# Performance work log

Hardware: AMD Instinct MI355X
Metric: run time of the kernel (lower is better)

The kernel has to match this reference:

```python
import jax, jax.numpy as jnp
import numpy as np

B, T, HID = 2, 1024, 1024
H, DK, DV = 16, 64, 64
K = 4            # short conv kernel size
CG = 15          # CG iterations (max_cg_step_training)
EPS = 1e-5       # norm_eps


def setup_inputs() -> dict:
    key = jax.random.key(0)
    ks = jax.random.split(key, 12)
    s = 1.0 / np.sqrt(HID)
    nrm = lambda k, sh, sc: (jax.random.normal(k, sh, jnp.float32) * sc)
    hidden_states = nrm(ks[0], (B, T, HID), 1.0)
    Wq = nrm(ks[1], (HID, HID), s)
    Wk = nrm(ks[2], (HID, HID), s)
    Wv = nrm(ks[3], (HID, HID), s)
    Wa = nrm(ks[4], (HID, H), s)
    Wb = nrm(ks[5], (HID, H), s)
    bb = jnp.zeros((H,), jnp.float32)
    A_log = jnp.log(jax.random.uniform(ks[6], (H,), jnp.float32, 1e-3, 16.0))
    dt = jnp.exp(jax.random.uniform(ks[7], (H,), jnp.float32) * (np.log(0.1) - np.log(0.001)) + np.log(0.001))
    dt = jnp.clip(dt, 1e-4)
    dt_bias = dt + jnp.log(-jnp.expm1(-dt))
    lam_init = float(np.log(np.exp(1.0 - 0.25) - 1.0))
    lambda_params = jnp.full((HID,), lam_init, jnp.float32)
    Wconv_q = nrm(ks[8], (HID, K), 0.3)
    Wconv_k = nrm(ks[9], (HID, K), 0.3)
    norm_w = jnp.ones((DV,), jnp.float32)
    Wo = nrm(ks[10], (HID, HID), s)
    return dict(hidden_states=hidden_states, Wq=Wq, Wk=Wk, Wv=Wv, Wa=Wa, Wb=Wb, bb=bb,
                A_log=A_log, dt_bias=dt_bias, lambda_params=lambda_params,
                Wconv_q=Wconv_q, Wconv_k=Wconv_k, norm_w=norm_w, Wo=Wo)


def _short_conv(x, w):
    # causal depthwise conv1d + silu. x: [b,t,c], w: [c,K]
    t = x.shape[1]
    xp = jnp.pad(x, ((0, 0), (K - 1, 0), (0, 0)))
    y = sum(xp[:, i:i + t, :] * w[:, i] for i in range(K))
    return jax.nn.silu(y)


def _l2norm(x):
    return x * jax.lax.rsqrt(jnp.sum(x * x, -1, keepdims=True) + 1e-6)


def _forward(hidden_states, Wq, Wk, Wv, Wa, Wb, bb, A_log, dt_bias, lambda_params, Wconv_q, Wconv_k, norm_w, Wo):
    b, t, _ = hidden_states.shape
    q = _short_conv(hidden_states @ Wq, Wconv_q)
    k = _short_conv(hidden_states @ Wk, Wconv_k)
    v = hidden_states @ Wv
    q = _l2norm(q.reshape(b, t, H, DK))
    k = _l2norm(k.reshape(b, t, H, DK))
    v = v.reshape(b, t, H, DV)
    beta = jax.nn.sigmoid(hidden_states @ Wb + bb)                         # [b,t,h]
    g = -jnp.exp(A_log) * jax.nn.softplus(hidden_states @ Wa + dt_bias)    # [b,t,h]
    lamb = jax.nn.softplus(lambda_params).reshape(H, DK) + 0.25            # [h,dk]

    def cg_solve(Hkk, rhs):
        # solve (Hkk + diag(lamb)) x = rhs, fixed-iteration CG, batched over [b,h]
        mv = lambda p: jnp.einsum('bhij,bhj->bhi', Hkk, p) + lamb * p
        x = jnp.zeros_like(rhs)
        r = rhs
        p = r
        rs = jnp.sum(r * r, -1, keepdims=True)
        for _ in range(CG):
            Ap = mv(p)
            alpha = rs / (jnp.sum(p * Ap, -1, keepdims=True) + 1e-12)
            x = x + alpha * p
            r = r - alpha * Ap
            rs_new = jnp.sum(r * r, -1, keepdims=True)
            p = r + (rs_new / (rs + 1e-12)) * p
            rs = rs_new
        return x

    def step(carry, inp):
        Hkk, Hkv = carry
        qt, kt, vt, gt, bt = inp
        decay = jnp.exp(gt)[..., None, None]
        w = bt[..., None, None]
        Hkk = decay * Hkk + w * (kt[..., :, None] * kt[..., None, :])
        Hkv = decay * Hkv + w * (kt[..., :, None] * vt[..., None, :])
        x = cg_solve(Hkk, qt)
        o = jnp.einsum('bhi,bhij->bhj', x, Hkv)
        return (Hkk, Hkv), o

    qT = q.transpose(1, 0, 2, 3)
    kT = k.transpose(1, 0, 2, 3)
    vT = v.transpose(1, 0, 2, 3)
    gT = g.transpose(1, 0, 2)
    bT = beta.transpose(1, 0, 2)
    Hkk0 = jnp.zeros((b, H, DK, DK), hidden_states.dtype)
    Hkv0 = jnp.zeros((b, H, DK, DV), hidden_states.dtype)
    _, oT = jax.lax.scan(jax.checkpoint(step), (Hkk0, Hkv0), (qT, kT, vT, gT, bT))
    o = oT.transpose(1, 0, 2, 3)                                           # [b,t,h,dv]
    o = o * jax.lax.rsqrt(jnp.mean(o * o, -1, keepdims=True) + EPS) * norm_w
    return o.reshape(b, t, H * DV) @ Wo


def reference(hidden_states, Wq, Wk, Wv, Wa, Wb, bb, A_log, dt_bias, lambda_params, Wconv_q, Wconv_k, norm_w, Wo):
    return _forward(hidden_states, Wq, Wk, Wv, Wa, Wb, bb, A_log, dt_bias, lambda_params, Wconv_q, Wconv_k, norm_w, Wo)
```

## Files before the change

kernel.cpp:

```cpp
#include <hip/hip_runtime.h>
#include <hip/hip_bf16.h>
#include <stdint.h>

#define T_LEN 1024
#define HIDN  1024
#define NH    16
#define DKV   64
#define KCONV 4
#define CG_IT 15
#define CC    32
#define NC    (T_LEN / CC)
#define PAD   68

typedef __attribute__((ext_vector_type(8))) short          bf16x8;
typedef __attribute__((ext_vector_type(8))) unsigned short u16x8;
typedef __attribute__((ext_vector_type(4))) unsigned short u16x4;
typedef __attribute__((ext_vector_type(4))) float          f32x4;

__device__ __forceinline__ float softplusf(float x) {
    return x > 20.f ? x : log1pf(expf(x));
}
__device__ __forceinline__ unsigned short f2bf(float x) {
    __hip_bfloat16 b = __float2bfloat16(x);
    return *reinterpret_cast<unsigned short*>(&b);
}
__device__ __forceinline__ bf16x8 pack8(float4 a, float4 b) {
    union { bf16x8 v; unsigned short u[8]; } r;
    r.u[0] = f2bf(a.x); r.u[1] = f2bf(a.y); r.u[2] = f2bf(a.z); r.u[3] = f2bf(a.w);
    r.u[4] = f2bf(b.x); r.u[5] = f2bf(b.y); r.u[6] = f2bf(b.z); r.u[7] = f2bf(b.w);
    return r.v;
}

__global__ __launch_bounds__(256) void cast_bf16(const float* __restrict__ src,
                                                 unsigned short* __restrict__ dst,
                                                 int n4)
{
    int i = blockIdx.x * 256 + threadIdx.x;
    if (i >= n4) return;
    float4 v = *reinterpret_cast<const float4*>(src + (size_t)i * 4);
    u16x4 o;
    o.x = f2bf(v.x); o.y = f2bf(v.y); o.z = f2bf(v.z); o.w = f2bf(v.w);
    *reinterpret_cast<u16x4*>(dst + (size_t)i * 4) = o;
}

__global__ __launch_bounds__(256) void transpose_cast(const float* __restrict__ W,
                                                      unsigned short* __restrict__ WT,
                                                      int K, int N)
{
    __shared__ unsigned short sT[64][68];
    int n0 = blockIdx.x * 64, k0 = blockIdx.y * 64;
    int tid = threadIdx.x;
    int rr = tid >> 4, cc4 = (tid & 15) * 4;
#pragma unroll
    for (int p = 0; p < 4; p++) {
        int r = p * 16 + rr;
        float4 v = *reinterpret_cast<const float4*>(&W[(size_t)(k0 + r) * N + n0 + cc4]);
        sT[cc4 + 0][r] = f2bf(v.x);
        sT[cc4 + 1][r] = f2bf(v.y);
        sT[cc4 + 2][r] = f2bf(v.z);
        sT[cc4 + 3][r] = f2bf(v.w);
    }
    __syncthreads();
#pragma unroll
    for (int p = 0; p < 4; p++) {
        int r = p * 16 + rr;
        u16x4 v = *reinterpret_cast<const u16x4*>(&sT[r][cc4]);
        *reinterpret_cast<u16x4*>(&WT[(size_t)(n0 + r) * K + k0 + cc4]) = v;
    }
}

__global__ __launch_bounds__(256) void gemm_bf16(const unsigned short* __restrict__ A,
                                                 const unsigned short* __restrict__ Bt,
                                                 float* __restrict__ C,
                                                 int M, int N, int K)
{
    __shared__ unsigned short sA[64][40];
    __shared__ unsigned short sB[64][40];
    const int tid = threadIdx.x;
    const int bm = blockIdx.y * 64, bn = blockIdx.x * 64;
    const int w = tid >> 6, lane = tid & 63;
    const int l16 = lane & 15, quad = lane >> 4;
    const int lrow = tid >> 2, lk = (tid & 3) * 8;

    f32x4 acc[4];
#pragma unroll
    for (int f = 0; f < 4; f++) acc[f] = (f32x4){0.f, 0.f, 0.f, 0.f};

    const size_t arow = (size_t)(bm + lrow) * K;
    const size_t brow = (size_t)(bn + lrow) * K;

    for (int k0 = 0; k0 < K; k0 += 32) {
        u16x8 av = *reinterpret_cast<const u16x8*>(A + arow + k0 + lk);
        u16x8 bv = *reinterpret_cast<const u16x8*>(Bt + brow + k0 + lk);
        *reinterpret_cast<u16x8*>(&sA[lrow][lk]) = av;
        *reinterpret_cast<u16x8*>(&sB[lrow][lk]) = bv;
        __syncthreads();

        bf16x8 aF = *reinterpret_cast<const bf16x8*>(&sA[w * 16 + l16][quad * 8]);
#pragma unroll
        for (int f = 0; f < 4; f++) {
            bf16x8 bF = *reinterpret_cast<const bf16x8*>(&sB[f * 16 + l16][quad * 8]);
            acc[f] = __builtin_amdgcn_mfma_f32_16x16x32_bf16(aF, bF, acc[f], 0, 0, 0);
        }
        __syncthreads();
    }

#pragma unroll
    for (int f = 0; f < 4; f++) {
#pragma unroll
        for (int i = 0; i < 4; i++) {
            int m = bm + w * 16 + quad * 4 + i;
            C[(size_t)m * N + bn + f * 16 + l16] = acc[f][i];
        }
    }
}

__global__ __launch_bounds__(256) void gemm_qkv(const unsigned short* __restrict__ A,
                                                const unsigned short* __restrict__ Bt,
                                                float* __restrict__ C)
{
    const int K = 1024;
    __shared__ unsigned short sA[64][40];
    __shared__ unsigned short sB[64][40];
    const int tid = threadIdx.x;
    const int bm = blockIdx.y * 64, bn = blockIdx.x * 64;
    const int mat = bn >> 10, n0 = bn & 1023;
    const int w = tid >> 6, lane = tid & 63;
    const int l16 = lane & 15, quad = lane >> 4;
    const int lrow = tid >> 2, lk = (tid & 3) * 8;

    f32x4 acc[4];
#pragma unroll
    for (int f = 0; f < 4; f++) acc[f] = (f32x4){0.f, 0.f, 0.f, 0.f};

    const size_t arow = (size_t)(bm + lrow) * K;
    const size_t brow = (size_t)(bn + lrow) * K;

    for (int k0 = 0; k0 < K; k0 += 32) {
        u16x8 av = *reinterpret_cast<const u16x8*>(A + arow + k0 + lk);
        u16x8 bv = *reinterpret_cast<const u16x8*>(Bt + brow + k0 + lk);
        *reinterpret_cast<u16x8*>(&sA[lrow][lk]) = av;
        *reinterpret_cast<u16x8*>(&sB[lrow][lk]) = bv;
        __syncthreads();

        bf16x8 aF = *reinterpret_cast<const bf16x8*>(&sA[w * 16 + l16][quad * 8]);
#pragma unroll
        for (int f = 0; f < 4; f++) {
            bf16x8 bF = *reinterpret_cast<const bf16x8*>(&sB[f * 16 + l16][quad * 8]);
            acc[f] = __builtin_amdgcn_mfma_f32_16x16x32_bf16(aF, bF, acc[f], 0, 0, 0);
        }
        __syncthreads();
    }

    float* Cb = C + (size_t)mat * (2048u * 1024u);
#pragma unroll
    for (int f = 0; f < 4; f++) {
#pragma unroll
        for (int i = 0; i < 4; i++) {
            int m = bm + w * 16 + quad * 4 + i;
            Cb[(size_t)m * 1024 + n0 + f * 16 + l16] = acc[f][i];
        }
    }
}

__global__ __launch_bounds__(256) void proj_gb(const float* __restrict__ hidden,
                                               const float* __restrict__ Wa,
                                               const float* __restrict__ Wb,
                                               const float* __restrict__ bb,
                                               const float* __restrict__ A_log,
                                               const float* __restrict__ dt_bias,
                                               float* __restrict__ g_out,
                                               float* __restrict__ beta_out)
{
    int idx = blockIdx.x * 256 + threadIdx.x;
    int row = idx >> 4, h = idx & 15;
    const float* hr = hidden + (size_t)row * HIDN;
    float da = 0.f, db = 0.f;
    for (int i = 0; i < HIDN; i++) {
        float x = hr[i];
        da += x * Wa[i * NH + h];
        db += x * Wb[i * NH + h];
    }
    float sp = softplusf(da + dt_bias[h]);
    g_out[idx]    = -expf(A_log[h]) * sp;
    beta_out[idx] = 1.f / (1.f + expf(-(db + bb[h])));
}

__global__ __launch_bounds__(1024) void cumsum_g(const float* __restrict__ g_in,
                                                 const float* __restrict__ beta_in,
                                                 float* __restrict__ G_out,
                                                 float* __restrict__ betaT)
{
    __shared__ float s[1024];
    int bh = blockIdx.x;
    int b = bh >> 4, h = bh & 15;
    int t = threadIdx.x;
    size_t src = ((size_t)(b * T_LEN) + t) * NH + h;
    s[t] = g_in[src];
    float bt = beta_in[src];
    __syncthreads();
    for (int off = 1; off < 1024; off <<= 1) {
        float tmp = (t >= off) ? s[t - off] : 0.f;
        __syncthreads();
        s[t] += tmp;
        __syncthreads();
    }
    G_out[(size_t)bh * T_LEN + t] = s[t];
    betaT[(size_t)bh * T_LEN + t] = bt;
}

__global__ __launch_bounds__(256) void conv_silu_l2(const float* __restrict__ pre,
                                                    const float* __restrict__ Wc,
                                                    float* __restrict__ out)
{
    int gid = blockIdx.x * 4 + (threadIdx.x >> 6);
    int lane = threadIdx.x & 63;
    int h = gid & 15;
    int t = (gid >> 4) & (T_LEN - 1);
    int b = gid >> 14;
    int c = h * DKV + lane;
    float acc = 0.f;
#pragma unroll
    for (int i = 0; i < KCONV; i++) {
        int ts = t - (KCONV - 1) + i;
        if (ts >= 0)
            acc += pre[((size_t)(b * T_LEN) + ts) * HIDN + c] * Wc[c * KCONV + i];
    }
    float y = acc / (1.f + expf(-acc));
    float ss = y * y;
#pragma unroll
    for (int m = 1; m < 64; m <<= 1) ss += __shfl_xor(ss, m);
    out[((size_t)(b * T_LEN) + t) * HIDN + c] = y * rsqrtf(ss + 1e-6f);
}

__global__ __launch_bounds__(256) void chunk_local(const float* __restrict__ kbuf,
                                                   const float* __restrict__ vbuf,
                                                   const float* __restrict__ G,
                                                   const float* __restrict__ betaT,
                                                   float* __restrict__ Akk,
                                                   float* __restrict__ AkvT)
{
    __shared__ float sK[CC][PAD];
    __shared__ float sV[CC][PAD];
    __shared__ float sW[CC];
    int bid = blockIdx.x;
    int half = bid & 1;
    int cidx = bid >> 1;
    int chunk = cidx & (NC - 1), bh = cidx >> 5;
    int b = bh >> 4, h = bh & 15;
    int tid = threadIdx.x;
    int i = half * 32 + (tid >> 3);
    int j0 = (tid & 7) * 8;
    int ls = tid >> 3, ld = (tid & 7) * 8;
    int t0 = chunk * CC;

    {
        size_t ga = (((size_t)(b * T_LEN) + t0 + ls) * NH + h) * 64 + ld;
        *reinterpret_cast<float4*>(&sK[ls][ld])     = *reinterpret_cast<const float4*>(&kbuf[ga]);
        *reinterpret_cast<float4*>(&sK[ls][ld + 4]) = *reinterpret_cast<const float4*>(&kbuf[ga + 4]);
        *reinterpret_cast<float4*>(&sV[ls][ld])     = *reinterpret_cast<const float4*>(&vbuf[ga]);
        *reinterpret_cast<float4*>(&sV[ls][ld + 4]) = *reinterpret_cast<const float4*>(&vbuf[ga + 4]);
        if (tid < CC) {
            float gv = G[(size_t)bh * T_LEN + t0 + tid];
            float bv = betaT[(size_t)bh * T_LEN + t0 + tid];
            float gend = __shfl(gv, 31);
            sW[tid] = expf(gend - gv) * bv;
        }
    }
    __syncthreads();

    float akk[8], akv[8];
#pragma unroll
    for (int j = 0; j < 8; j++) { akk[j] = 0.f; akv[j] = 0.f; }
#pragma unroll 4
    for (int s = 0; s < CC; s++) {
        float wk = sW[s] * sK[s][i];
        float wv = sW[s] * sV[s][i];
        float4 ka = *reinterpret_cast<const float4*>(&sK[s][j0]);
        float4 kb = *reinterpret_cast<const float4*>(&sK[s][j0 + 4]);
        akk[0] += wk * ka.x; akk[1] += wk * ka.y; akk[2] += wk * ka.z; akk[3] += wk * ka.w;
        akk[4] += wk * kb.x; akk[5] += wk * kb.y; akk[6] += wk * kb.z; akk[7] += wk * kb.w;
        akv[0] += wv * ka.x; akv[1] += wv * ka.y; akv[2] += wv * ka.z; akv[3] += wv * ka.w;
        akv[4] += wv * kb.x; akv[5] += wv * kb.y; akv[6] += wv * kb.z; akv[7] += wv * kb.w;
    }
    size_t ob = ((size_t)cidx * 64 + i) * 64 + j0;
    *reinterpret_cast<float4*>(&Akk[ob])      = make_float4(akk[0], akk[1], akk[2], akk[3]);
    *reinterpret_cast<float4*>(&Akk[ob + 4])  = make_float4(akk[4], akk[5], akk[6], akk[7]);
    *reinterpret_cast<float4*>(&AkvT[ob])     = make_float4(akv[0], akv[1], akv[2], akv[3]);
    *reinterpret_cast<float4*>(&AkvT[ob + 4]) = make_float4(akv[4], akv[5], akv[6], akv[7]);
}

__global__ __launch_bounds__(256) void chunk_prefix(float* __restrict__ Hkk,
                                                    float* __restrict__ HkvT,
                                                    const float* __restrict__ G)
{
    __shared__ float sDec[NC];
    int blk = blockIdx.x;
    int bh = blk >> 3, sub = blk & 7;
    int tid = threadIdx.x;
    if (tid < NC)
        sDec[tid] = (tid > 0)
            ? expf(G[(size_t)bh * T_LEN + tid * CC + CC - 1] - G[(size_t)bh * T_LEN + tid * CC - 1])
            : 1.f;
    __syncthreads();
    int flat = sub * 256 + tid;
    int mat = flat >> 10, e4 = flat & 1023;
    float* base = (mat ? HkvT : Hkk) + (size_t)bh * NC * 4096 + (size_t)e4 * 4;
    float4 state = make_float4(0.f, 0.f, 0.f, 0.f);
#pragma unroll 1
    for (int c = 0; c < NC; c++) {
        float4* p = reinterpret_cast<float4*>(base + (size_t)c * 4096);
        float4 a = *p;
        *p = state;
        float d = sDec[c];
        state.x = d * state.x + a.x;
        state.y = d * state.y + a.y;
        state.z = d * state.z + a.z;
        state.w = d * state.w + a.w;
    }
}

__global__ __launch_bounds__(256, 1) void scan_mfma(
    const float* __restrict__ qbuf, const float* __restrict__ kbuf,
    const float* __restrict__ vbuf, const float* __restrict__ G,
    const float* __restrict__ betaT, const float* __restrict__ Hkk0,
    const float* __restrict__ HkvT0, const float* __restrict__ lambda_p,
    const float* __restrict__ norm_w, unsigned short* __restrict__ obf)
{
    __shared__ __align__(16) unsigned short sP[4][32][72];
    __shared__ __align__(16) unsigned short sM[4][32][40];

    const int tid = threadIdx.x;
    const int wv = tid >> 6, lane = tid & 63;
    const int quad = lane >> 4, l16 = lane & 15;
    const int W = blockIdx.x * 4 + wv;
    const int bh = W >> 5, chunk = W & 31;
    const int b = bh >> 4, h = bh & 15;
    const int t0 = chunk * CC;
    unsigned short (*sPw)[72] = sP[wv];
    unsigned short (*sMw)[40] = sM[wv];

    const size_t rbase = ((size_t)(b * T_LEN + t0) * NH + h) * 64;
    const float* Gb = G + (size_t)bh * T_LEN + t0;
    const float* Bb = betaT + (size_t)bh * T_LEN + t0;
    const float Gprev = (chunk > 0) ? Gb[-1] : 0.f;

    float Gt[2][4], et[2][4];
#pragma unroll
    for (int tm = 0; tm < 2; tm++)
#pragma unroll
        for (int reg = 0; reg < 4; reg++) {
            float g = Gb[16 * tm + 4 * quad + reg];
            Gt[tm][reg] = g;
            et[tm][reg] = expf(g - Gprev);
        }
    float Co[2][2][4];
#pragma unroll
    for (int sn = 0; sn < 2; sn++) {
        int s = 16 * sn + l16;
        float Gs = Gb[s], bts = Bb[s];
#pragma unroll
        for (int tm = 0; tm < 2; tm++)
#pragma unroll
            for (int reg = 0; reg < 4; reg++) {
                int t = 16 * tm + 4 * quad + reg;
                Co[tm][sn][reg] = (s <= t) ? expf(Gt[tm][reg] - Gs) * bts : 0.f;
            }
    }
    float lam[4], nw[4];
#pragma unroll
    for (int f = 0; f < 4; f++) {
        lam[f] = softplusf(lambda_p[h * 64 + 16 * f + l16]) + 0.25f;
        nw[f]  = norm_w[16 * f + l16];
    }

    bf16x8 Kb[2][2];
#pragma unroll
    for (int sn = 0; sn < 2; sn++) {
        const float* kr = kbuf + rbase + (size_t)(16 * sn + l16) * 1024;
#pragma unroll
        for (int ks = 0; ks < 2; ks++) {
            float4 a = *reinterpret_cast<const float4*>(kr + 8 * quad + 32 * ks);
            float4 c = *reinterpret_cast<const float4*>(kr + 8 * quad + 32 * ks + 4);
            Kb[sn][ks] = pack8(a, c);
        }
    }
    bf16x8 KTb[4];
#pragma unroll
    for (int f = 0; f < 4; f++) {
        union { bf16x8 v; unsigned short u[8]; } r;
#pragma unroll
        for (int j = 0; j < 8; j++)
            r.u[j] = f2bf(kbuf[rbase + (size_t)(8 * quad + j) * 1024 + 16 * f + l16]);
        KTb[f] = r.v;
    }
    const size_t hbase = ((size_t)(bh * NC) + chunk) * 4096;
    bf16x8 Hb[4][2];
#pragma unroll
    for (int f = 0; f < 4; f++) {
        const float* hr = Hkk0 + hbase + (size_t)(16 * f + l16) * 64;
#pragma unroll
        for (int ks = 0; ks < 2; ks++) {
            float4 a = *reinterpret_cast<const float4*>(hr + 8 * quad + 32 * ks);
            float4 c = *reinterpret_cast<const float4*>(hr + 8 * quad + 32 * ks + 4);
            Hb[f][ks] = pack8(a, c);
        }
    }

    f32x4 X[2][4], R[2][4], P[2][4];
    float rs8[2][4];
#pragma unroll
    for (int tm = 0; tm < 2; tm++)
#pragma unroll
        for (int reg = 0; reg < 4; reg++) rs8[tm][reg] = 0.f;
#pragma unroll
    for (int tm = 0; tm < 2; tm++)
#pragma unroll
        for (int f = 0; f < 4; f++) {
#pragma unroll
            for (int reg = 0; reg < 4; reg++) {
                float q = qbuf[rbase + (size_t)(16 * tm + 4 * quad + reg) * 1024 + 16 * f + l16];
                P[tm][f][reg] = q; R[tm][f][reg] = q; X[tm][f][reg] = 0.f;
                rs8[tm][reg] += q * q;
            }
        }
#pragma unroll
    for (int tm = 0; tm < 2; tm++)
#pragma unroll
        for (int reg = 0; reg < 4; reg++) {
            float v = rs8[tm][reg];
            v += __shfl_xor(v, 1); v += __shfl_xor(v, 2);
            v += __shfl_xor(v, 4); v += __shfl_xor(v, 8);
            rs8[tm][reg] = v;
        }

    const f32x4 zero4 = {0.f, 0.f, 0.f, 0.f};

#pragma unroll 1
    for (int it = 0; it < CG_IT; it++) {
#pragma unroll
        for (int tm = 0; tm < 2; tm++)
#pragma unroll
            for (int reg = 0; reg < 4; reg++)
#pragma unroll
                for (int f = 0; f < 4; f++)
                    sPw[16 * tm + 4 * quad + reg][16 * f + l16] = f2bf(P[tm][f][reg]);
        __threadfence_block();
        bf16x8 Pa[2][2];
#pragma unroll
        for (int tm = 0; tm < 2; tm++)
#pragma unroll
            for (int ks = 0; ks < 2; ks++)
                Pa[tm][ks] = *reinterpret_cast<const bf16x8*>(&sPw[16 * tm + l16][8 * quad + 32 * ks]);
        f32x4 D[2][2];
#pragma unroll
        for (int tm = 0; tm < 2; tm++)
#pragma unroll
            for (int sn = 0; sn < 2; sn++) {
                f32x4 d = __builtin_amdgcn_mfma_f32_16x16x32_bf16(Pa[tm][0], Kb[sn][0], zero4, 0, 0, 0);
                D[tm][sn] = __builtin_amdgcn_mfma_f32_16x16x32_bf16(Pa[tm][1], Kb[sn][1], d, 0, 0, 0);
            }
#pragma unroll
        for (int tm = 0; tm < 2; tm++)
#pragma unroll
            for (int sn = 0; sn < 2; sn++)
#pragma unroll
                for (int reg = 0; reg < 4; reg++)
                    sMw[16 * tm + 4 * quad + reg][16 * sn + l16] = f2bf(Co[tm][sn][reg] * D[tm][sn][reg]);
        __threadfence_block();
        bf16x8 Ma[2];
#pragma unroll
        for (int tm = 0; tm < 2; tm++)
            Ma[tm] = *reinterpret_cast<const bf16x8*>(&sMw[16 * tm + l16][8 * quad]);
        f32x4 AP[2][4], A2[2][4];
#pragma unroll
        for (int tm = 0; tm < 2; tm++)
#pragma unroll
            for (int f = 0; f < 4; f++) {
                AP[tm][f] = __builtin_amdgcn_mfma_f32_16x16x32_bf16(Ma[tm], KTb[f], zero4, 0, 0, 0);
                f32x4 a = __builtin_amdgcn_mfma_f32_16x16x32_bf16(Pa[tm][0], Hb[f][0], zero4, 0, 0, 0);
                A2[tm][f] = __builtin_amdgcn_mfma_f32_16x16x32_bf16(Pa[tm][1], Hb[f][1], a, 0, 0, 0);
            }
#pragma unroll
        for (int tm = 0; tm < 2; tm++)
#pragma unroll
            for (int f = 0; f < 4; f++)
#pragma unroll
                for (int reg = 0; reg < 4; reg++)
                    AP[tm][f][reg] = lam[f] * P[tm][f][reg] + AP[tm][f][reg] + et[tm][reg] * A2[tm][f][reg];
        float alpha[2][4], rsn[2][4];
#pragma unroll
        for (int tm = 0; tm < 2; tm++)
#pragma unroll
            for (int reg = 0; reg < 4; reg++) {
                float s = 0.f;
#pragma unroll
                for (int f = 0; f < 4; f++) s += P[tm][f][reg] * AP[tm][f][reg];
                s += __shfl_xor(s, 1); s += __shfl_xor(s, 2);
                s += __shfl_xor(s, 4); s += __shfl_xor(s, 8);
                alpha[tm][reg] = rs8[tm][reg] / (s + 1e-12f);
                rsn[tm][reg] = 0.f;
            }
#pragma unroll
        for (int tm = 0; tm < 2; tm++)
#pragma unroll
            for (int f = 0; f < 4; f++)
#pragma unroll
                for (int reg = 0; reg < 4; reg++) {
                    X[tm][f][reg] += alpha[tm][reg] * P[tm][f][reg];
                    float rv = R[tm][f][reg] - alpha[tm][reg] * AP[tm][f][reg];
                    R[tm][f][reg] = rv;
                    rsn[tm][reg] += rv * rv;
                }
#pragma unroll
        for (int tm = 0; tm < 2; tm++)
#pragma unroll
            for (int reg = 0; reg < 4; reg++) {
                float v = rsn[tm][reg];
                v += __shfl_xor(v, 1); v += __shfl_xor(v, 2);
                v += __shfl_xor(v, 4); v += __shfl_xor(v, 8);
                float btac = v / (rs8[tm][reg] + 1e-12f);
                rs8[tm][reg] = v;
#pragma unroll
                for (int f = 0; f < 4; f++)
                    P[tm][f][reg] = R[tm][f][reg] + btac * P[tm][f][reg];
            }
    }

#pragma unroll
    for (int tm = 0; tm < 2; tm++)
#pragma unroll
        for (int reg = 0; reg < 4; reg++)
#pragma unroll
            for (int f = 0; f < 4; f++)
                sPw[16 * tm + 4 * quad + reg][16 * f + l16] = f2bf(X[tm][f][reg]);
    __threadfence_block();
    bf16x8 Xa[2][2];
#pragma unroll
    for (int tm = 0; tm < 2; tm++)
#pragma unroll
        for (int ks = 0; ks < 2; ks++)
            Xa[tm][ks] = *reinterpret_cast<const bf16x8*>(&sPw[16 * tm + l16][8 * quad + 32 * ks]);
    f32x4 Do[2][2];
#pragma unroll
    for (int tm = 0; tm < 2; tm++)
#pragma unroll
        for (int sn = 0; sn < 2; sn++) {
            f32x4 d = __builtin_amdgcn_mfma_f32_16x16x32_bf16(Xa[tm][0], Kb[sn][0], zero4, 0, 0, 0);
            Do[tm][sn] = __builtin_amdgcn_mfma_f32_16x16x32_bf16(Xa[tm][1], Kb[sn][1], d, 0, 0, 0);
        }
#pragma unroll
    for (int tm = 0; tm < 2; tm++)
#pragma unroll
        for (int sn = 0; sn < 2; sn++)
#pragma unroll
            for (int reg = 0; reg < 4; reg++)
                sMw[16 * tm + 4 * quad + reg][16 * sn + l16] = f2bf(Co[tm][sn][reg] * Do[tm][sn][reg]);
    __threadfence_block();
    bf16x8 Mo[2];
#pragma unroll
    for (int tm = 0; tm < 2; tm++)
        Mo[tm] = *reinterpret_cast<const bf16x8*>(&sMw[16 * tm + l16][8 * quad]);
    bf16x8 Vb[4];
#pragma unroll
    for (int f = 0; f < 4; f++) {
        union { bf16x8 v; unsigned short u[8]; } r;
#pragma unroll
        for (int j = 0; j < 8; j++)
            r.u[j] = f2bf(vbuf[rbase + (size_t)(8 * quad + j) * 1024 + 16 * f + l16]);
        Vb[f] = r.v;
    }
    bf16x8 Hvb[4][2];
#pragma unroll
    for (int f = 0; f < 4; f++) {
        const float* hr = HkvT0 + hbase + (size_t)(16 * f + l16) * 64;
#pragma unroll
        for (int ks = 0; ks < 2; ks++) {
            float4 a = *reinterpret_cast<const float4*>(hr + 8 * quad + 32 * ks);
            float4 c = *reinterpret_cast<const float4*>(hr + 8 * quad + 32 * ks + 4);
            Hvb[f][ks] = pack8(a, c);
        }
    }
    f32x4 O[2][4];
#pragma unroll
    for (int tm = 0; tm < 2; tm++)
#pragma unroll
        for (int f = 0; f < 4; f++) {
            f32x4 o1 = __builtin_amdgcn_mfma_f32_16x16x32_bf16(Mo[tm], Vb[f], zero4, 0, 0, 0);
            f32x4 o2 = __builtin_amdgcn_mfma_f32_16x16x32_bf16(Xa[tm][0], Hvb[f][0], zero4, 0, 0, 0);
            o2 = __builtin_amdgcn_mfma_f32_16x16x32_bf16(Xa[tm][1], Hvb[f][1], o2, 0, 0, 0);
#pragma unroll
            for (int reg = 0; reg < 4; reg++)
                O[tm][f][reg] = o1[reg] + et[tm][reg] * o2[reg];
        }
#pragma unroll
    for (int tm = 0; tm < 2; tm++)
#pragma unroll
        for (int reg = 0; reg < 4; reg++) {
            float s = 0.f;
#pragma unroll
            for (int f = 0; f < 4; f++) s += O[tm][f][reg] * O[tm][f][reg];
            s += __shfl_xor(s, 1); s += __shfl_xor(s, 2);
            s += __shfl_xor(s, 4); s += __shfl_xor(s, 8);
            float scale = rsqrtf(s * (1.f / 64.f) + 1e-5f);
            size_t orow = rbase + (size_t)(16 * tm + 4 * quad + reg) * 1024;
#pragma unroll
            for (int f = 0; f < 4; f++)
                obf[orow + 16 * f + l16] = f2bf(O[tm][f][reg] * scale * nw[f]);
        }
}

extern "C" void kernel_launch(void* const* d_in, const int* in_sizes, int n_in,
                              void* d_out, int out_size, void* d_ws, size_t ws_size,
                              hipStream_t stream)
{
    const float* hidden   = (const float*)d_in[0];
    const float* Wq       = (const float*)d_in[1];
    const float* Wk       = (const float*)d_in[2];
    const float* Wv       = (const float*)d_in[3];
    const float* Wa       = (const float*)d_in[4];
    const float* Wb       = (const float*)d_in[5];
    const float* bb       = (const float*)d_in[6];
    const float* A_log    = (const float*)d_in[7];
    const float* dt_bias  = (const float*)d_in[8];
    const float* lambda_p = (const float*)d_in[9];
    const float* Wconv_q  = (const float*)d_in[10];
    const float* Wconv_k  = (const float*)d_in[11];
    const float* norm_w   = (const float*)d_in[12];
    const float* Wo       = (const float*)d_in[13];
    float* out = (float*)d_out;

    float* ws = (float*)d_ws;
    const size_t SZ_BIG = (size_t)2 * T_LEN * HIDN;
    float* qpre = ws;
    float* kpre = qpre + SZ_BIG;
    float* vbuf = kpre + SZ_BIG;
    float* qbuf = vbuf + SZ_BIG;
    float* kbuf = qbuf + SZ_BIG;
    float* gbuf = kbuf + SZ_BIG;
    float* bbuf = gbuf + 32768;
    float* Gbuf = bbuf + 32768;
    float* btT  = Gbuf + 32768;
    float* Hkk0 = btT + 32768;
    float* HkvT0 = Hkk0 + (size_t)32 * NC * 4096;
    unsigned short* WoT = (unsigned short*)(HkvT0 + (size_t)32 * NC * 4096);

    unsigned short* hidden_bf = (unsigned short*)HkvT0;
    unsigned short* WqT = (unsigned short*)Hkk0;
    unsigned short* obuf_bf = (unsigned short*)kpre;

    const int M = 2 * T_LEN;

    cast_bf16<<<(M * HIDN / 4 + 255) / 256, 256, 0, stream>>>(hidden, hidden_bf, M * HIDN / 4);
    dim3 tg(HIDN / 64, HIDN / 64);
    transpose_cast<<<tg, 256, 0, stream>>>(Wq, WqT, HIDN, HIDN);
    transpose_cast<<<tg, 256, 0, stream>>>(Wk, WqT + (size_t)HIDN * HIDN, HIDN, HIDN);
    transpose_cast<<<tg, 256, 0, stream>>>(Wv, WqT + (size_t)2 * HIDN * HIDN, HIDN, HIDN);
    transpose_cast<<<tg, 256, 0, stream>>>(Wo, WoT, HIDN, HIDN);

    dim3 gq(3 * HIDN / 64, M / 64);
    gemm_qkv<<<gq, 256, 0, stream>>>(hidden_bf, WqT, qpre);
    proj_gb<<<128, 256, 0, stream>>>(hidden, Wa, Wb, bb, A_log, dt_bias, gbuf, bbuf);
    cumsum_g<<<32, 1024, 0, stream>>>(gbuf, bbuf, Gbuf, btT);
    conv_silu_l2<<<M * NH / 4, 256, 0, stream>>>(qpre, Wconv_q, qbuf);
    conv_silu_l2<<<M * NH / 4, 256, 0, stream>>>(kpre, Wconv_k, kbuf);
    chunk_local<<<2048, 256, 0, stream>>>(kbuf, vbuf, Gbuf, btT, Hkk0, HkvT0);
    chunk_prefix<<<256, 256, 0, stream>>>(Hkk0, HkvT0, Gbuf);
    scan_mfma<<<256, 256, 0, stream>>>(qbuf, kbuf, vbuf, Gbuf, btT, Hkk0, HkvT0,
                                       lambda_p, norm_w, obuf_bf);
    dim3 gg(HIDN / 64, M / 64);
    gemm_bf16<<<gg, 256, 0, stream>>>(obuf_bf, WoT, out, M, HIDN, HIDN);
}
```

Baseline: 304.8 us.

## Split scan rows across two waves and parallelize gate projection per row

The chunked CG scan now gives each 32-step chunk to two wavefronts, each handling 16 query rows, which doubles the grid and allows two blocks per CU so the serial CG loop has more parallel waves and fewer registers per wave. Separately, the g/beta projection moves from one thread per (row, head) looping over all 1024 inputs to one wavefront per row with vectorized loads and a cross-lane reduction. The scan split recomputes the K, H and coefficient loads in both waves, and the projection adds shuffle-reduction overhead.

```diff
diff --git a/kernel.cpp b/kernel.cpp
--- a/kernel.cpp
+++ b/kernel.cpp
@@ -172,18 +172,56 @@
                                                float* __restrict__ g_out,
                                                float* __restrict__ beta_out)
 {
-    int idx = blockIdx.x * 256 + threadIdx.x;
-    int row = idx >> 4, h = idx & 15;
-    const float* hr = hidden + (size_t)row * HIDN;
-    float da = 0.f, db = 0.f;
-    for (int i = 0; i < HIDN; i++) {
-        float x = hr[i];
-        da += x * Wa[i * NH + h];
-        db += x * Wb[i * NH + h];
-    }
-    float sp = softplusf(da + dt_bias[h]);
-    g_out[idx]    = -expf(A_log[h]) * sp;
-    beta_out[idx] = 1.f / (1.f + expf(-(db + bb[h])));
+    int wvid = threadIdx.x >> 6, lane = threadIdx.x & 63;
+    int row = blockIdx.x * 4 + wvid;
+    const float* hr = hidden + (size_t)row * HIDN + 16 * lane;
+    const float* war = Wa + (size_t)(16 * lane) * NH;
+    const float* wbr = Wb + (size_t)(16 * lane) * NH;
+
+    float da[16], db[16];
+#pragma unroll
+    for (int h = 0; h < 16; h++) { da[h] = 0.f; db[h] = 0.f; }
+
+#pragma unroll
+    for (int j = 0; j < 16; j += 4) {
+        float4 xv = *reinterpret_cast<const float4*>(hr + j);
+        float xs[4] = {xv.x, xv.y, xv.z, xv.w};
+#pragma unroll
+        for (int e = 0; e < 4; e++) {
+            int i = j + e;
+            float x = xs[e];
+            const float4* wa4 = reinterpret_cast<const float4*>(war + i * NH);
+            const float4* wb4 = reinterpret_cast<const float4*>(wbr + i * NH);
+#pragma unroll
+            for (int q = 0; q < 4; q++) {
+                float4 wa = wa4[q], wb = wb4[q];
+                da[q * 4 + 0] += x * wa.x; da[q * 4 + 1] += x * wa.y;
+                da[q * 4 + 2] += x * wa.z; da[q * 4 + 3] += x * wa.w;
+                db[q * 4 + 0] += x * wb.x; db[q * 4 + 1] += x * wb.y;
+                db[q * 4 + 2] += x * wb.z; db[q * 4 + 3] += x * wb.w;
+            }
+        }
+    }
+#pragma unroll
+    for (int m = 1; m < 64; m <<= 1) {
+#pragma unroll
+        for (int h = 0; h < 16; h++) {
+            da[h] += __shfl_xor(da[h], m);
+            db[h] += __shfl_xor(db[h], m);
+        }
+    }
+    float dah = 0.f, dbh = 0.f;
+#pragma unroll
+    for (int h = 0; h < 16; h++) {
+        bool sel = (lane == h);
+        dah = sel ? da[h] : dah;
+        dbh = sel ? db[h] : dbh;
+    }
+    if (lane < 16) {
+        float sp = softplusf(dah + dt_bias[lane]);
+        g_out[row * NH + lane]    = -expf(A_log[lane]) * sp;
+        beta_out[row * NH + lane] = 1.f / (1.f + expf(-(dbh + bb[lane])));
+    }
 }
 
 __global__ __launch_bounds__(1024) void cumsum_g(const float* __restrict__ g_in,
@@ -320,23 +358,26 @@
     }
 }
 
-__global__ __launch_bounds__(256, 1) void scan_mfma(
+__global__ __launch_bounds__(256, 2) void scan_mfma(
     const float* __restrict__ qbuf, const float* __restrict__ kbuf,
     const float* __restrict__ vbuf, const float* __restrict__ G,
     const float* __restrict__ betaT, const float* __restrict__ Hkk0,
     const float* __restrict__ HkvT0, const float* __restrict__ lambda_p,
     const float* __restrict__ norm_w, unsigned short* __restrict__ obf)
 {
-    __shared__ __align__(16) unsigned short sP[4][32][72];
-    __shared__ __align__(16) unsigned short sM[4][32][40];
+    __shared__ __align__(16) unsigned short sP[4][16][72];
+    __shared__ __align__(16) unsigned short sM[4][16][40];
 
     const int tid = threadIdx.x;
     const int wv = tid >> 6, lane = tid & 63;
     const int quad = lane >> 4, l16 = lane & 15;
     const int W = blockIdx.x * 4 + wv;
-    const int bh = W >> 5, chunk = W & 31;
+    const int half = W & 1;
+    const int cidx = W >> 1;
+    const int bh = cidx >> 5, chunk = cidx & 31;
     const int b = bh >> 4, h = bh & 15;
     const int t0 = chunk * CC;
+    const int rbofs = 16 * half + 4 * quad;
     unsigned short (*sPw)[72] = sP[wv];
     unsigned short (*sMw)[40] = sM[wv];
 
@@ -345,27 +386,23 @@
     const float* Bb = betaT + (size_t)bh * T_LEN + t0;
     const float Gprev = (chunk > 0) ? Gb[-1] : 0.f;
 
-    float Gt[2][4], et[2][4];
-#pragma unroll
-    for (int tm = 0; tm < 2; tm++)
-#pragma unroll
-        for (int reg = 0; reg < 4; reg++) {
-            float g = Gb[16 * tm + 4 * quad + reg];
-            Gt[tm][reg] = g;
-            et[tm][reg] = expf(g - Gprev);
-        }
-    float Co[2][2][4];
+    float Gt[4], et[4];
+#pragma unroll
+    for (int reg = 0; reg < 4; reg++) {
+        float g = Gb[rbofs + reg];
+        Gt[reg] = g;
+        et[reg] = expf(g - Gprev);
+    }
+    float Co[2][4];
 #pragma unroll
     for (int sn = 0; sn < 2; sn++) {
         int s = 16 * sn + l16;
         float Gs = Gb[s], bts = Bb[s];
 #pragma unroll
-        for (int tm = 0; tm < 2; tm++)
-#pragma unroll
-            for (int reg = 0; reg < 4; reg++) {
-                int t = 16 * tm + 4 * quad + reg;
-                Co[tm][sn][reg] = (s <= t) ? expf(Gt[tm][reg] - Gs) * bts : 0.f;
-            }
+        for (int reg = 0; reg < 4; reg++) {
+            int t = rbofs + reg;
+            Co[sn][reg] = (s <= t) ? expf(Gt[reg] - Gs) * bts : 0.f;
+        }
     }
     float lam[4], nw[4];
 #pragma unroll
@@ -407,160 +444,122 @@
         }
     }
 
-    f32x4 X[2][4], R[2][4], P[2][4];
-    float rs8[2][4];
-#pragma unroll
-    for (int tm = 0; tm < 2; tm++)
-#pragma unroll
-        for (int reg = 0; reg < 4; reg++) rs8[tm][reg] = 0.f;
-#pragma unroll
-    for (int tm = 0; tm < 2; tm++)
+    f32x4 X[4], R[4], P[4];
+    float rs8[4];
+#pragma unroll
+    for (int reg = 0; reg < 4; reg++) rs8[reg] = 0.f;
+#pragma unroll
+    for (int f = 0; f < 4; f++) {
+#pragma unroll
+        for (int reg = 0; reg < 4; reg++) {
+            float q = qbuf[rbase + (size_t)(rbofs + reg) * 1024 + 16 * f + l16];
+            P[f][reg] = q; R[f][reg] = q; X[f][reg] = 0.f;
+            rs8[reg] += q * q;
+        }
+    }
+#pragma unroll
+    for (int reg = 0; reg < 4; reg++) {
+        float v = rs8[reg];
+        v += __shfl_xor(v, 1); v += __shfl_xor(v, 2);
+        v += __shfl_xor(v, 4); v += __shfl_xor(v, 8);
+        rs8[reg] = v;
+    }
+
+    const f32x4 zero4 = {0.f, 0.f, 0.f, 0.f};
+
+#pragma unroll 1
+    for (int it = 0; it < CG_IT; it++) {
+#pragma unroll
+        for (int reg = 0; reg < 4; reg++)
+#pragma unroll
+            for (int f = 0; f < 4; f++)
+                sPw[4 * quad + reg][16 * f + l16] = f2bf(P[f][reg]);
+        __threadfence_block();
+        bf16x8 Pa[2];
+#pragma unroll
+        for (int ks = 0; ks < 2; ks++)
+            Pa[ks] = *reinterpret_cast<const bf16x8*>(&sPw[l16][8 * quad + 32 * ks]);
+        f32x4 D[2];
+#pragma unroll
+        for (int sn = 0; sn < 2; sn++) {
+            f32x4 d = __builtin_amdgcn_mfma_f32_16x16x32_bf16(Pa[0], Kb[sn][0], zero4, 0, 0, 0);
+            D[sn] = __builtin_amdgcn_mfma_f32_16x16x32_bf16(Pa[1], Kb[sn][1], d, 0, 0, 0);
+        }
+#pragma unroll
+        for (int sn = 0; sn < 2; sn++)
+#pragma unroll
+            for (int reg = 0; reg < 4; reg++)
+                sMw[4 * quad + reg][16 * sn + l16] = f2bf(Co[sn][reg] * D[sn][reg]);
+        __threadfence_block();
+        bf16x8 Ma = *reinterpret_cast<const bf16x8*>(&sMw[l16][8 * quad]);
+        f32x4 AP[4], A2[4];
 #pragma unroll
         for (int f = 0; f < 4; f++) {
+            AP[f] = __builtin_amdgcn_mfma_f32_16x16x32_bf16(Ma, KTb[f], zero4, 0, 0, 0);
+            f32x4 a = __builtin_amdgcn_mfma_f32_16x16x32_bf16(Pa[0], Hb[f][0], zero4, 0, 0, 0);
+            A2[f] = __builtin_amdgcn_mfma_f32_16x16x32_bf16(Pa[1], Hb[f][1], a, 0, 0, 0);
+        }
+#pragma unroll
+        for (int f = 0; f < 4; f++)
+#pragma unroll
+            for (int reg = 0; reg < 4; reg++)
+                AP[f][reg] = lam[f] * P[f][reg] + AP[f][reg] + et[reg] * A2[f][reg];
+        float alpha[4], rsn[4];
+#pragma unroll
+        for (int reg = 0; reg < 4; reg++) {
+            float s = 0.f;
+#pragma unroll
+            for (int f = 0; f < 4; f++) s += P[f][reg] * AP[f][reg];
+            s += __shfl_xor(s, 1); s += __shfl_xor(s, 2);
+            s += __shfl_xor(s, 4); s += __shfl_xor(s, 8);
+            alpha[reg] = rs8[reg] / (s + 1e-12f);
+            rsn[reg] = 0.f;
+        }
+#pragma unroll
+        for (int f = 0; f < 4; f++)
 #pragma unroll
             for (int reg = 0; reg < 4; reg++) {
-                float q = qbuf[rbase + (size_t)(16 * tm + 4 * quad + reg) * 1024 + 16 * f + l16];
-                P[tm][f][reg] = q; R[tm][f][reg] = q; X[tm][f][reg] = 0.f;
-                rs8[tm][reg] += q * q;
+                X[f][reg] += alpha[reg] * P[f][reg];
+                float rv = R[f][reg] - alpha[reg] * AP[f][reg];
+                R[f][reg] = rv;
+                rsn[reg] += rv * rv;
             }
-        }
-#pragma unroll
-    for (int tm = 0; tm < 2; tm++)
 #pragma unroll
         for (int reg = 0; reg < 4; reg++) {
-            float v = rs8[tm][reg];
+            float v = rsn[reg];
             v += __shfl_xor(v, 1); v += __shfl_xor(v, 2);
             v += __shfl_xor(v, 4); v += __shfl_xor(v, 8);
-            rs8[tm][reg] = v;
-        }
-
-    const f32x4 zero4 = {0.f, 0.f, 0.f, 0.f};
-
-#pragma unroll 1
-    for (int it = 0; it < CG_IT; it++) {
-#pragma unroll
-        for (int tm = 0; tm < 2; tm++)
-#pragma unroll
-            for (int reg = 0; reg < 4; reg++)
-#pragma unroll
-                for (int f = 0; f < 4; f++)
-                    sPw[16 * tm + 4 * quad + reg][16 * f + l16] = f2bf(P[tm][f][reg]);
-        __threadfence_block();
-        bf16x8 Pa[2][2];
-#pragma unroll
-        for (int tm = 0; tm < 2; tm++)
-#pragma unroll
-            for (int ks = 0; ks < 2; ks++)
-                Pa[tm][ks] = *reinterpret_cast<const bf16x8*>(&sPw[16 * tm + l16][8 * quad + 32 * ks]);
-        f32x4 D[2][2];
-#pragma unroll
-        for (int tm = 0; tm < 2; tm++)
-#pragma unroll
-            for (int sn = 0; sn < 2; sn++) {
-                f32x4 d = __builtin_amdgcn_mfma_f32_16x16x32_bf16(Pa[tm][0], Kb[sn][0], zero4, 0, 0, 0);
-                D[tm][sn] = __builtin_amdgcn_mfma_f32_16x16x32_bf16(Pa[tm][1], Kb[sn][1], d, 0, 0, 0);
-            }
-#pragma unroll
-        for (int tm = 0; tm < 2; tm++)
-#pragma unroll
-            for (int sn = 0; sn < 2; sn++)
-#pragma unroll
-                for (int reg = 0; reg < 4; reg++)
-                    sMw[16 * tm + 4 * quad + reg][16 * sn + l16] = f2bf(Co[tm][sn][reg] * D[tm][sn][reg]);
-        __threadfence_block();
-        bf16x8 Ma[2];
-#pragma unroll
-        for (int tm = 0; tm < 2; tm++)
-            Ma[tm] = *reinterpret_cast<const bf16x8*>(&sMw[16 * tm + l16][8 * quad]);
-        f32x4 AP[2][4], A2[2][4];
-#pragma unroll
-        for (int tm = 0; tm < 2; tm++)
-#pragma unroll
-            for (int f = 0; f < 4; f++) {
-                AP[tm][f] = __builtin_amdgcn_mfma_f32_16x16x32_bf16(Ma[tm], KTb[f], zero4, 0, 0, 0);
-                f32x4 a = __builtin_amdgcn_mfma_f32_16x16x32_bf16(Pa[tm][0], Hb[f][0], zero4, 0, 0, 0);
-                A2[tm][f] = __builtin_amdgcn_mfma_f32_16x16x32_bf16(Pa[tm][1], Hb[f][1], a, 0, 0, 0);
-            }
-#pragma unroll
-        for (int tm = 0; tm < 2; tm++)
+            float btac = v / (rs8[reg] + 1e-12f);
+            rs8[reg] = v;
 #pragma unroll
             for (int f = 0; f < 4; f++)
-#pragma unroll
-                for (int reg = 0; reg < 4; reg++)
-                    AP[tm][f][reg] = lam[f] * P[tm][f][reg] + AP[tm][f][reg] + et[tm][reg] * A2[tm][f][reg];
-        float alpha[2][4], rsn[2][4];
-#pragma unroll
-        for (int tm = 0; tm < 2; tm++)
-#pragma unroll
-            for (int reg = 0; reg < 4; reg++) {
-                float s = 0.f;
-#pragma unroll
-                for (int f = 0; f < 4; f++) s += P[tm][f][reg] * AP[tm][f][reg];
-                s += __shfl_xor(s, 1); s += __shfl_xor(s, 2);
-                s += __shfl_xor(s, 4); s += __shfl_xor(s, 8);
-                alpha[tm][reg] = rs8[tm][reg] / (s + 1e-12f);
-                rsn[tm][reg] = 0.f;
-            }
-#pragma unroll
-        for (int tm = 0; tm < 2; tm++)
-#pragma unroll
-            for (int f = 0; f < 4; f++)
-#pragma unroll
-                for (int reg = 0; reg < 4; reg++) {
-                    X[tm][f][reg] += alpha[tm][reg] * P[tm][f][reg];
-                    float rv = R[tm][f][reg] - alpha[tm][reg] * AP[tm][f][reg];
-                    R[tm][f][reg] = rv;
-                    rsn[tm][reg] += rv * rv;
-                }
-#pragma unroll
-        for (int tm = 0; tm < 2; tm++)
-#pragma unroll
-            for (int reg = 0; reg < 4; reg++) {
-                float v = rsn[tm][reg];
-                v += __shfl_xor(v, 1); v += __shfl_xor(v, 2);
-                v += __shfl_xor(v, 4); v += __shfl_xor(v, 8);
-                float btac = v / (rs8[tm][reg] + 1e-12f);
-                rs8[tm][reg] = v;
-#pragma unroll
-                for (int f = 0; f < 4; f++)
-                    P[tm][f][reg] = R[tm][f][reg] + btac * P[tm][f][reg];
-            }
-    }
-
-#pragma unroll
-    for (int tm = 0; tm < 2; tm++)
+                P[f][reg] = R[f][reg] + btac * P[f][reg];
+        }
+    }
+
+#pragma unroll
+    for (int reg = 0; reg < 4; reg++)
+#pragma unroll
+        for (int f = 0; f < 4; f++)
+            sPw[4 * quad + reg][16 * f + l16] = f2bf(X[f][reg]);
+    __threadfence_block();
+    bf16x8 Xa[2];
+#pragma unroll
+    for (int ks = 0; ks < 2; ks++)
+        Xa[ks] = *reinterpret_cast<const bf16x8*>(&sPw[l16][8 * quad + 32 * ks]);
+    f32x4 Do[2];
+#pragma unroll
+    for (int sn = 0; sn < 2; sn++) {
+        f32x4 d = __builtin_amdgcn_mfma_f32_16x16x32_bf16(Xa[0], Kb[sn][0], zero4, 0, 0, 0);
+        Do[sn] = __builtin_amdgcn_mfma_f32_16x16x32_bf16(Xa[1], Kb[sn][1], d, 0, 0, 0);
+    }
+#pragma unroll
+    for (int sn = 0; sn < 2; sn++)
 #pragma unroll
         for (int reg = 0; reg < 4; reg++)
-#pragma unroll
-            for (int f = 0; f < 4; f++)
-                sPw[16 * tm + 4 * quad + reg][16 * f + l16] = f2bf(X[tm][f][reg]);
+            sMw[4 * quad + reg][16 * sn + l16] = f2bf(Co[sn][reg] * Do[sn][reg]);
     __threadfence_block();
-    bf16x8 Xa[2][2];
-#pragma unroll
-    for (int tm = 0; tm < 2; tm++)
-#pragma unroll
-        for (int ks = 0; ks < 2; ks++)
-            Xa[tm][ks] = *reinterpret_cast<const bf16x8*>(&sPw[16 * tm + l16][8 * quad + 32 * ks]);
-    f32x4 Do[2][2];
-#pragma unroll
-    for (int tm = 0; tm < 2; tm++)
-#pragma unroll
-        for (int sn = 0; sn < 2; sn++) {
-            f32x4 d = __builtin_amdgcn_mfma_f32_16x16x32_bf16(Xa[tm][0], Kb[sn][0], zero4, 0, 0, 0);
-            Do[tm][sn] = __builtin_amdgcn_mfma_f32_16x16x32_bf16(Xa[tm][1], Kb[sn][1], d, 0, 0, 0);
-        }
-#pragma unroll
-    for (int tm = 0; tm < 2; tm++)
-#pragma unroll
-        for (int sn = 0; sn < 2; sn++)
-#pragma unroll
-            for (int reg = 0; reg < 4; reg++)
-                sMw[16 * tm + 4 * quad + reg][16 * sn + l16] = f2bf(Co[tm][sn][reg] * Do[tm][sn][reg]);
-    __threadfence_block();
-    bf16x8 Mo[2];
-#pragma unroll
-    for (int tm = 0; tm < 2; tm++)
-        Mo[tm] = *reinterpret_cast<const bf16x8*>(&sMw[16 * tm + l16][8 * quad]);
+    bf16x8 Mo = *reinterpret_cast<const bf16x8*>(&sMw[l16][8 * quad]);
     bf16x8 Vb[4];
 #pragma unroll
     for (int f = 0; f < 4; f++) {
@@ -581,33 +580,29 @@
             Hvb[f][ks] = pack8(a, c);
         }
     }
-    f32x4 O[2][4];
-#pragma unroll
-    for (int tm = 0; tm < 2; tm++)
-#pragma unroll
-        for (int f = 0; f < 4; f++) {
-            f32x4 o1 = __builtin_amdgcn_mfma_f32_16x16x32_bf16(Mo[tm], Vb[f], zero4, 0, 0, 0);
-            f32x4 o2 = __builtin_amdgcn_mfma_f32_16x16x32_bf16(Xa[tm][0], Hvb[f][0], zero4, 0, 0, 0);
-            o2 = __builtin_amdgcn_mfma_f32_16x16x32_bf16(Xa[tm][1], Hvb[f][1], o2, 0, 0, 0);
-#pragma unroll
-            for (int reg = 0; reg < 4; reg++)
-                O[tm][f][reg] = o1[reg] + et[tm][reg] * o2[reg];
-        }
-#pragma unroll
-    for (int tm = 0; tm < 2; tm++)
-#pragma unroll
-        for (int reg = 0; reg < 4; reg++) {
-            float s = 0.f;
-#pragma unroll
-            for (int f = 0; f < 4; f++) s += O[tm][f][reg] * O[tm][f][reg];
-            s += __shfl_xor(s, 1); s += __shfl_xor(s, 2);
-            s += __shfl_xor(s, 4); s += __shfl_xor(s, 8);
-            float scale = rsqrtf(s * (1.f / 64.f) + 1e-5f);
-            size_t orow = rbase + (size_t)(16 * tm + 4 * quad + reg) * 1024;
-#pragma unroll
-            for (int f = 0; f < 4; f++)
-                obf[orow + 16 * f + l16] = f2bf(O[tm][f][reg] * scale * nw[f]);
-        }
+    f32x4 O[4];
+#pragma unroll
+    for (int f = 0; f < 4; f++) {
+        f32x4 o1 = __builtin_amdgcn_mfma_f32_16x16x32_bf16(Mo, Vb[f], zero4, 0, 0, 0);
+        f32x4 o2 = __builtin_amdgcn_mfma_f32_16x16x32_bf16(Xa[0], Hvb[f][0], zero4, 0, 0, 0);
+        o2 = __builtin_amdgcn_mfma_f32_16x16x32_bf16(Xa[1], Hvb[f][1], o2, 0, 0, 0);
+#pragma unroll
+        for (int reg = 0; reg < 4; reg++)
+            O[f][reg] = o1[reg] + et[reg] * o2[reg];
+    }
+#pragma unroll
+    for (int reg = 0; reg < 4; reg++) {
+        float s = 0.f;
+#pragma unroll
+        for (int f = 0; f < 4; f++) s += O[f][reg] * O[f][reg];
+        s += __shfl_xor(s, 1); s += __shfl_xor(s, 2);
+        s += __shfl_xor(s, 4); s += __shfl_xor(s, 8);
+        float scale = rsqrtf(s * (1.f / 64.f) + 1e-5f);
+        size_t orow = rbase + (size_t)(rbofs + reg) * 1024;
+#pragma unroll
+        for (int f = 0; f < 4; f++)
+            obf[orow + 16 * f + l16] = f2bf(O[f][reg] * scale * nw[f]);
+    }
 }
 
 extern "C" void kernel_launch(void* const* d_in, const int* in_sizes, int n_in,
@@ -660,13 +655,13 @@
 
     dim3 gq(3 * HIDN / 64, M / 64);
     gemm_qkv<<<gq, 256, 0, stream>>>(hidden_bf, WqT, qpre);
-    proj_gb<<<128, 256, 0, stream>>>(hidden, Wa, Wb, bb, A_log, dt_bias, gbuf, bbuf);
+    proj_gb<<<M / 4, 256, 0, stream>>>(hidden, Wa, Wb, bb, A_log, dt_bias, gbuf, bbuf);
     cumsum_g<<<32, 1024, 0, stream>>>(gbuf, bbuf, Gbuf, btT);
     conv_silu_l2<<<M * NH / 4, 256, 0, stream>>>(qpre, Wconv_q, qbuf);
     conv_silu_l2<<<M * NH / 4, 256, 0, stream>>>(kpre, Wconv_k, kbuf);
     chunk_local<<<2048, 256, 0, stream>>>(kbuf, vbuf, Gbuf, btT, Hkk0, HkvT0);
     chunk_prefix<<<256, 256, 0, stream>>>(Hkk0, HkvT0, Gbuf);
-    scan_mfma<<<256, 256, 0, stream>>>(qbuf, kbuf, vbuf, Gbuf, btT, Hkk0, HkvT0,
+    scan_mfma<<<512, 256, 0, stream>>>(qbuf, kbuf, vbuf, Gbuf, btT, Hkk0, HkvT0,
                                        lambda_p, norm_w, obuf_bf);
     dim3 gg(HIDN / 64, M / 64);
     gemm_bf16<<<gg, 256, 0, stream>>>(obuf_bf, WoT, out, M, HIDN, HIDN);
```

Result: faster. 284.4 us (-6.7%).
